# Kernel tuning notes

Hardware: AMD Instinct MI355X
Metric: run time of the kernel (lower is better)

The kernel has to match this reference:

```python
import jax, jax.numpy as jnp
import numpy as np

ANCHORS = np.array([[10.,13.],[16.,30.],[33.,23.],[30.,61.],[62.,45.],
                    [59.,119.],[116.,90.],[156.,198.],[373.,326.]], dtype=np.float32)
ANCHOR_MASK = [[6,7,8],[3,4,5],[0,1,2]]
INPUT_WH = np.array([320., 320.], dtype=np.float32)  # (W, H) == input_shape[::-1] (square)
IGNORE_THRESH = 0.5
NUM_CLASSES = 80
GRIDS = [10, 20, 40]
BATCH = 4


def _bce_logits(labels, logits):
    # tf.nn.sigmoid_cross_entropy_with_logits
    return jnp.maximum(logits, 0.0) - logits * labels + jnp.log1p(jnp.exp(-jnp.abs(logits)))


def _yolo_head(feats, anchors):
    gh, gw = feats.shape[1], feats.shape[2]
    gx = jnp.arange(gw, dtype=feats.dtype)
    gy = jnp.arange(gh, dtype=feats.dtype)
    # grid[..., 0] = x, grid[..., 1] = y ; shape [gh, gw, 1, 2]
    grid = jnp.stack(jnp.meshgrid(gx, gy), axis=-1)[:, :, None, :]
    box_xy = (jax.nn.sigmoid(feats[..., :2]) + grid) / jnp.array([gw, gh], feats.dtype)
    anc = jnp.asarray(anchors, feats.dtype).reshape(1, 1, 1, -1, 2)
    box_wh = jnp.exp(feats[..., 2:4]) * anc / jnp.asarray(INPUT_WH, feats.dtype)
    return grid, box_xy, box_wh


def _pairwise_iou(p, t):
    # p: [B,P,4] pred boxes (cx,cy,w,h); t: [B,N,4] true boxes -> iou [B,P,N]
    p_min = p[:, :, None, :2] - p[:, :, None, 2:4] * 0.5
    p_max = p[:, :, None, :2] + p[:, :, None, 2:4] * 0.5
    t_min = t[:, None, :, :2] - t[:, None, :, 2:4] * 0.5
    t_max = t[:, None, :, :2] + t[:, None, :, 2:4] * 0.5
    wh = jnp.maximum(jnp.minimum(p_max, t_max) - jnp.maximum(p_min, t_min), 0.0)
    inter = wh[..., 0] * wh[..., 1]
    p_area = p[:, :, None, 2] * p[:, :, None, 3]
    t_area = t[:, None, :, 2] * t[:, None, :, 3]
    return inter / (p_area + t_area - inter)


def _layer_loss(t, y, anchors, g):
    obj = t[..., 4:5]                      # [B,g,g,3,1]
    objb = obj != 0
    grid, pxy, pwh = _yolo_head(y, anchors)
    pred_box = jnp.concatenate([pxy, pwh], axis=-1)
    raw_true_xy = t[..., :2] * jnp.array([g, g], t.dtype) - grid
    anc = jnp.asarray(anchors, t.dtype).reshape(1, 1, 1, -1, 2)
    wh_scaled = t[..., 2:4] * jnp.asarray(INPUT_WH, t.dtype) / anc
    raw_true_wh = jnp.where(objb, jnp.log(jnp.where(objb, wh_scaled, 1.0)), 0.0)
    box_scale = 2.0 - t[..., 2:3] * t[..., 3:4]

    # ignore mask: masked pairwise IoU (all-slots, statically shaped; mask = objectness)
    B = t.shape[0]
    P = g * g * 3
    pb = pred_box.reshape(B, P, 4)
    tb = t[..., :4].reshape(B, P, 4)
    tmask = (t[..., 4] != 0).reshape(B, P)
    iou = _pairwise_iou(pb, tb)                         # [B,P,P]
    iou = jnp.where(tmask[:, None, :], iou, -jnp.inf)
    best_iou = jnp.max(iou, axis=-1)                    # -inf when no true boxes (matches empty reduce_max)
    ignore = (best_iou < IGNORE_THRESH).astype(t.dtype).reshape(obj.shape)

    xy_loss = obj * box_scale * _bce_logits(raw_true_xy, y[..., 0:2])
    wh_loss = obj * box_scale * 0.5 * jnp.square(raw_true_wh - y[..., 2:4])
    conf_loss = (obj + (1.0 - obj) * ignore) * _bce_logits(obj, y[..., 4:5])
    cls_loss = obj * _bce_logits(t[..., 5:], y[..., 5:])

    per_img = (xy_loss.sum((1, 2, 3, 4)) + wh_loss.sum((1, 2, 3, 4))
               + conf_loss.sum((1, 2, 3, 4)) + cls_loss.sum((1, 2, 3, 4)))
    return jnp.mean(per_img)


def setup_inputs() -> dict:
    key = jax.random.key(0)
    inp = {}
    for l, g in enumerate(GRIDS):
        k = jax.random.fold_in(key, l)
        k1, k2, k3, k4, k5 = jax.random.split(k, 5)
        xy = jax.random.uniform(k1, (BATCH, g, g, 3, 2), jnp.float32)
        wh = jax.random.uniform(k2, (BATCH, g, g, 3, 2), jnp.float32, 0.05, 0.9)
        obj = jax.random.bernoulli(k3, 0.02, (BATCH, g, g, 3, 1)).astype(jnp.float32)
        cls = jax.random.uniform(k4, (BATCH, g, g, 3, NUM_CLASSES), jnp.float32)
        inp[f"t{l}"] = jnp.concatenate([xy, wh, obj, cls], axis=-1)
        inp[f"y{l}"] = jax.random.normal(k5, (BATCH, g, g, 3, 5 + NUM_CLASSES), jnp.float32)
    return inp


def reference(t0, t1, t2, y0, y1, y2):
    targets = [t0, t1, t2]
    outputs = [y0, y1, y2]
    loss = jnp.float32(0.0)
    for l in range(3):
        loss = loss + _layer_loss(targets[l], outputs[l], ANCHORS[ANCHOR_MASK[l]], GRIDS[l])
    return loss
```

## Files before the change

kernel.cpp:

```cpp
#include <hip/hip_runtime.h>
#include <math.h>


#define NBLK 104
#define SCAP 512
#define NT4 535500

__device__ __constant__ float c_anc[3][3][2] = {
  {{116.f, 90.f}, {156.f, 198.f}, {373.f, 326.f}},
  {{ 30.f, 61.f}, { 62.f,  45.f}, { 59.f, 119.f}},
  {{ 10.f, 13.f}, { 16.f,  30.f}, { 33.f,  23.f}}};

__device__ __forceinline__ float bce_f(float label, float logit) {
    return fmaxf(logit, 0.0f) - logit * label + log1pf(expf(-fabsf(logit)));
}

__global__ __launch_bounds__(256) void k_scan(
    const float* __restrict__ t0, const float* __restrict__ y0,
    const float* __restrict__ t1, const float* __restrict__ y1,
    const float* __restrict__ t2, const float* __restrict__ y2,
    float* __restrict__ flag, float4* __restrict__ boxes,
    float* __restrict__ qbuf, int* __restrict__ done)
{
    int gid = blockIdx.x * 256 + threadIdx.x;
    if (gid == 0) *done = 0;
    int stride = gridDim.x * 256;
    for (int i = gid; i < 2 * NT4; i += stride) {
        bool isY = i >= NT4;
        int f4 = isY ? i - NT4 : i;
        const float* src; int rowBase, fi;
        if (f4 < 25500)       { src = isY ? y0 : t0; fi = f4 * 4;              rowBase = 0;    }
        else if (f4 < 127500) { src = isY ? y1 : t1; fi = (f4 - 25500) * 4;    rowBase = 1200; }
        else                  { src = isY ? y2 : t2; fi = (f4 - 127500) * 4;   rowBase = 6000; }
        float4 v = *(const float4*)(src + fi);
        float xs[4] = {v.x, v.y, v.z, v.w};
        #pragma unroll
        for (int c = 0; c < 4; ++c) {
            int f = fi + c;
            int row = f / 85;
            int ch  = f - row * 85;
            float x = xs[c];
            int grow = rowBase + row;
            if (!isY) {
                if (ch == 4) {
                    flag[grow] = x;
                    if (x != 0.0f) {
                        const float* tp = src + (size_t)row * 85;
                        boxes[grow] = make_float4(tp[0], tp[1], tp[2], tp[3]);
                    }
                }
            } else {
                if (ch < 5) qbuf[grow * 5 + ch] = x;
            }
        }
    }
}

template<int P, int G>
__device__ __forceinline__ float layer_block(
    const float* __restrict__ t, const float* __restrict__ y,
    int img, int chunk, int rowBase, const float (*anc)[2],
    const float* __restrict__ flag, const float4* __restrict__ boxes,
    const float* __restrict__ qbuf,
    float4* sbox, int* scount)
{
    const int gbase = rowBase + img * P;
    const float* fimg = flag + gbase;

    if (threadIdx.x == 0) *scount = 0;
    __syncthreads();
    const float4* fimg4 = (const float4*)fimg;
    for (int k4 = threadIdx.x; k4 < P / 4; k4 += 256) {
        float4 fv = fimg4[k4];
        float fs[4] = {fv.x, fv.y, fv.z, fv.w};
        #pragma unroll
        for (int c = 0; c < 4; ++c) {
            if (fs[c] != 0.0f) {
                int off = atomicAdd(scount, 1);
                if (off < SCAP) sbox[off] = boxes[gbase + k4 * 4 + c];
            }
        }
    }
    __syncthreads();
    int cnt = *scount; if (cnt > SCAP) cnt = SCAP;
    int cntPad = (cnt + 7) & ~7;
    for (int k = cnt + threadIdx.x; k < cntPad; k += 256)
        sbox[k] = make_float4(0.f, 0.f, 0.f, 0.f);
    __syncthreads();

    int pos = chunk * 256 + threadIdx.x;
    bool valid = pos < P;
    float acc = 0.0f, obj = 0.0f;
    if (valid) {
        const float* qp = qbuf + (size_t)(gbase + pos) * 5;
        float q0 = qp[0], q1 = qp[1], q2 = qp[2], q3 = qp[3], q4 = qp[4];
        obj = fimg[pos];
        int a = pos % 3, cell = pos / 3;
        int j = cell % G, i = cell / G;
        float aw = anc[a][0], ah = anc[a][1];
        float gi = (float)G;

        float px = (1.0f / (1.0f + expf(-q0)) + (float)j) / gi;
        float py = (1.0f / (1.0f + expf(-q1)) + (float)i) / gi;
        float pw = expf(q2) * aw * (1.0f / 320.0f);
        float ph = expf(q3) * ah * (1.0f / 320.0f);
        float phx = pw * 0.5f, phy = ph * 0.5f;
        float pminx = px - phx, pmaxx = px + phx;
        float pminy = py - phy, pmaxy = py + phy;
        float parea = pw * ph;

        float best = -INFINITY;
        for (int k0 = 0; k0 < cntPad; k0 += 8) {
            #pragma unroll
            for (int u = 0; u < 8; ++u) {
                float4 tb = sbox[k0 + u];
                float thx = tb.z * 0.5f, thy = tb.w * 0.5f;
                float wx = fminf(pmaxx, tb.x + thx) - fmaxf(pminx, tb.x - thx);
                float wy = fminf(pmaxy, tb.y + thy) - fmaxf(pminy, tb.y - thy);
                wx = fmaxf(wx, 0.0f);
                wy = fmaxf(wy, 0.0f);
                float inter = wx * wy;
                float iou = inter / (parea + tb.z * tb.w - inter);
                best = fmaxf(best, iou);
            }
        }
        float ignore = (best < 0.5f) ? 1.0f : 0.0f;
        float bce_c = fmaxf(q4, 0.0f) - q4 * obj + log1pf(expf(-fabsf(q4)));
        acc = (obj + (1.0f - obj) * ignore) * bce_c;
    }

    const float* tslab = t + (size_t)img * P * 85;
    const float* yslab = y + (size_t)img * P * 85;
    unsigned long long m = __ballot(valid && obj != 0.0f);
    int lane = threadIdx.x & 63;
    int waveBase = chunk * 256 + (threadIdx.x & ~63);
    while (m) {
        int b = __ffsll(m) - 1; m &= m - 1;
        int ppos = waveBase + b;
        const float* tp = tslab + (size_t)ppos * 85;
        const float* yp = yslab + (size_t)ppos * 85;
        float tv1 = tp[lane], yv1 = yp[lane];
        bool has2 = lane < 21;
        float tv2 = 0.f, yv2 = 0.f;
        if (has2) { tv2 = tp[lane + 64]; yv2 = yp[lane + 64]; }

        float tw = __shfl(tv1, 2, 64);
        float th = __shfl(tv1, 3, 64);
        float bs = 2.0f - tw * th;
        int a = ppos % 3, cell = ppos / 3;
        int jj = cell % G, ii = cell / G;
        float aw = anc[a][0], ah = anc[a][1];

        float term;
        if (lane == 0)      term = bs * bce_f(tv1 * (float)G - (float)jj, yv1);
        else if (lane == 1) term = bs * bce_f(tv1 * (float)G - (float)ii, yv1);
        else if (lane == 2) { float d = logf(tv1 * 320.0f / aw) - yv1; term = bs * 0.5f * d * d; }
        else if (lane == 3) { float d = logf(tv1 * 320.0f / ah) - yv1; term = bs * 0.5f * d * d; }
        else if (lane == 4) term = 0.0f;
        else                term = bce_f(tv1, yv1);
        if (has2) term += bce_f(tv2, yv2);
        acc += term;
    }
    return acc;
}

__global__ __launch_bounds__(256) void k_main(
    const float* __restrict__ t0, const float* __restrict__ y0,
    const float* __restrict__ t1, const float* __restrict__ y1,
    const float* __restrict__ t2, const float* __restrict__ y2,
    const float* __restrict__ flag, const float4* __restrict__ boxes,
    const float* __restrict__ qbuf,
    float* __restrict__ partials, int* __restrict__ done,
    float* __restrict__ out)
{
    __shared__ float4 sbox[SCAP];
    __shared__ int scount;
    int blk = blockIdx.x;

    float acc;
    if (blk < 8)       acc = layer_block< 300, 10>(t0, y0, blk >> 1, blk & 1, 0, c_anc[0], flag, boxes, qbuf, sbox, &scount);
    else if (blk < 28) { int r = blk - 8;  acc = layer_block<1200, 20>(t1, y1, r / 5,  r % 5,  1200, c_anc[1], flag, boxes, qbuf, sbox, &scount); }
    else               { int r = blk - 28; acc = layer_block<4800, 40>(t2, y2, r / 19, r % 19, 6000, c_anc[2], flag, boxes, qbuf, sbox, &scount); }

    float v = acc;
    #pragma unroll
    for (int o = 32; o > 0; o >>= 1) v += __shfl_down(v, o, 64);
    __shared__ float red[4];
    int lane = threadIdx.x & 63, w = threadIdx.x >> 6;
    if (lane == 0) red[w] = v;
    __syncthreads();

    if (threadIdx.x < 64) {
        int old = 0;
        if (threadIdx.x == 0) {
            float p = ((red[0] + red[1]) + (red[2] + red[3])) * 0.25f;
            __hip_atomic_store(&partials[blk], p, __ATOMIC_RELAXED, __HIP_MEMORY_SCOPE_AGENT);
            old = __hip_atomic_fetch_add(done, 1, __ATOMIC_ACQ_REL, __HIP_MEMORY_SCOPE_AGENT);
        }
        old = __shfl(old, 0, 64);
        if (old == NBLK - 1) {
            float s = 0.0f;
            if (lane < NBLK - 64)
                s = __hip_atomic_load(&partials[lane + 64], __ATOMIC_RELAXED, __HIP_MEMORY_SCOPE_AGENT);
            s += __hip_atomic_load(&partials[lane], __ATOMIC_RELAXED, __HIP_MEMORY_SCOPE_AGENT);
            #pragma unroll
            for (int o = 32; o > 0; o >>= 1) s += __shfl_down(s, o, 64);
            if (lane == 0) out[0] = s;
        }
    }
}

extern "C" void kernel_launch(void* const* d_in, const int* in_sizes, int n_in,
                              void* d_out, int out_size, void* d_ws, size_t ws_size,
                              hipStream_t stream) {
    const float* t0 = (const float*)d_in[0];
    const float* y0 = (const float*)d_in[1];
    const float* t1 = (const float*)d_in[2];
    const float* y1 = (const float*)d_in[3];
    const float* t2 = (const float*)d_in[4];
    const float* y2 = (const float*)d_in[5];

    float*  flag     = (float*)d_ws;
    float4* boxes    = (float4*)((char*)d_ws + 102400);
    float*  qbuf     = (float*)((char*)d_ws + 512000);
    float*  partials = (float*)((char*)d_ws + 1016064);
    int*    done     = (int*)((char*)d_ws + 1020160);
    float*  out      = (float*)d_out;

    k_scan<<<2048, 256, 0, stream>>>(t0, y0, t1, y1, t2, y2, flag, boxes, qbuf, done);
    k_main<<<NBLK, 256, 0, stream>>>(t0, y0, t1, y1, t2, y2, flag, boxes, qbuf, partials, done, out);
}
```

Baseline: 34.57 us.

## Fuse scan and main kernels into one cooperative launch with grid sync

Merges the scan pass and the loss pass into a single cooperative kernel of 512 blocks, separated by a grid-wide barrier, with only the first 104 blocks continuing into the loss phase. This removes one kernel launch and the inter-kernel gap. In exchange it adds cooperative-launch overhead and a grid barrier, and the scan now runs on 512 blocks instead of 2048.

```diff
diff --git a/kernel.cpp b/kernel.cpp
--- a/kernel.cpp
+++ b/kernel.cpp
@@ -1,10 +1,14 @@
 #include <hip/hip_runtime.h>
+#include <hip/hip_cooperative_groups.h>
 #include <math.h>
+
+namespace cg = cooperative_groups;
 
 
 #define NBLK 104
 #define SCAP 512
 #define NT4 535500
+#define GRID_BLOCKS 512
 
 __device__ __constant__ float c_anc[3][3][2] = {
   {{116.f, 90.f}, {156.f, 198.f}, {373.f, 326.f}},
@@ -15,16 +19,126 @@
     return fmaxf(logit, 0.0f) - logit * label + log1pf(expf(-fabsf(logit)));
 }
 
-__global__ __launch_bounds__(256) void k_scan(
+template<int P, int G>
+__device__ __forceinline__ float layer_block(
+    const float* __restrict__ t, const float* __restrict__ y,
+    int img, int chunk, int rowBase, const float (*anc)[2],
+    const float* __restrict__ flag, const float4* __restrict__ boxes,
+    const float* __restrict__ qbuf,
+    float4* sbox, int* scount)
+{
+    const int gbase = rowBase + img * P;
+    const float* fimg = flag + gbase;
+
+    if (threadIdx.x == 0) *scount = 0;
+    __syncthreads();
+    const float4* fimg4 = (const float4*)fimg;
+    for (int k4 = threadIdx.x; k4 < P / 4; k4 += 256) {
+        float4 fv = fimg4[k4];
+        float fs[4] = {fv.x, fv.y, fv.z, fv.w};
+        #pragma unroll
+        for (int c = 0; c < 4; ++c) {
+            if (fs[c] != 0.0f) {
+                int off = atomicAdd(scount, 1);
+                if (off < SCAP) sbox[off] = boxes[gbase + k4 * 4 + c];
+            }
+        }
+    }
+    __syncthreads();
+    int cnt = *scount; if (cnt > SCAP) cnt = SCAP;
+    int cntPad = (cnt + 7) & ~7;
+    for (int k = cnt + threadIdx.x; k < cntPad; k += 256)
+        sbox[k] = make_float4(0.f, 0.f, 0.f, 0.f);
+    __syncthreads();
+
+    int pos = chunk * 256 + threadIdx.x;
+    bool valid = pos < P;
+    float acc = 0.0f, obj = 0.0f;
+    if (valid) {
+        const float* qp = qbuf + (size_t)(gbase + pos) * 5;
+        float q0 = qp[0], q1 = qp[1], q2 = qp[2], q3 = qp[3], q4 = qp[4];
+        obj = fimg[pos];
+        int a = pos % 3, cell = pos / 3;
+        int j = cell % G, i = cell / G;
+        float aw = anc[a][0], ah = anc[a][1];
+        float gi = (float)G;
+
+        float px = (1.0f / (1.0f + expf(-q0)) + (float)j) / gi;
+        float py = (1.0f / (1.0f + expf(-q1)) + (float)i) / gi;
+        float pw = expf(q2) * aw * (1.0f / 320.0f);
+        float ph = expf(q3) * ah * (1.0f / 320.0f);
+        float phx = pw * 0.5f, phy = ph * 0.5f;
+        float pminx = px - phx, pmaxx = px + phx;
+        float pminy = py - phy, pmaxy = py + phy;
+        float parea = pw * ph;
+
+        float best = -INFINITY;
+        for (int k0 = 0; k0 < cntPad; k0 += 8) {
+            #pragma unroll
+            for (int u = 0; u < 8; ++u) {
+                float4 tb = sbox[k0 + u];
+                float thx = tb.z * 0.5f, thy = tb.w * 0.5f;
+                float wx = fminf(pmaxx, tb.x + thx) - fmaxf(pminx, tb.x - thx);
+                float wy = fminf(pmaxy, tb.y + thy) - fmaxf(pminy, tb.y - thy);
+                wx = fmaxf(wx, 0.0f);
+                wy = fmaxf(wy, 0.0f);
+                float inter = wx * wy;
+                float iou = inter / (parea + tb.z * tb.w - inter);
+                best = fmaxf(best, iou);
+            }
+        }
+        float ignore = (best < 0.5f) ? 1.0f : 0.0f;
+        float bce_c = fmaxf(q4, 0.0f) - q4 * obj + log1pf(expf(-fabsf(q4)));
+        acc = (obj + (1.0f - obj) * ignore) * bce_c;
+    }
+
+    const float* tslab = t + (size_t)img * P * 85;
+    const float* yslab = y + (size_t)img * P * 85;
+    unsigned long long m = __ballot(valid && obj != 0.0f);
+    int lane = threadIdx.x & 63;
+    int waveBase = chunk * 256 + (threadIdx.x & ~63);
+    while (m) {
+        int b = __ffsll(m) - 1; m &= m - 1;
+        int ppos = waveBase + b;
+        const float* tp = tslab + (size_t)ppos * 85;
+        const float* yp = yslab + (size_t)ppos * 85;
+        float tv1 = tp[lane], yv1 = yp[lane];
+        bool has2 = lane < 21;
+        float tv2 = 0.f, yv2 = 0.f;
+        if (has2) { tv2 = tp[lane + 64]; yv2 = yp[lane + 64]; }
+
+        float tw = __shfl(tv1, 2, 64);
+        float th = __shfl(tv1, 3, 64);
+        float bs = 2.0f - tw * th;
+        int a = ppos % 3, cell = ppos / 3;
+        int jj = cell % G, ii = cell / G;
+        float aw = anc[a][0], ah = anc[a][1];
+
+        float term;
+        if (lane == 0)      term = bs * bce_f(tv1 * (float)G - (float)jj, yv1);
+        else if (lane == 1) term = bs * bce_f(tv1 * (float)G - (float)ii, yv1);
+        else if (lane == 2) { float d = logf(tv1 * 320.0f / aw) - yv1; term = bs * 0.5f * d * d; }
+        else if (lane == 3) { float d = logf(tv1 * 320.0f / ah) - yv1; term = bs * 0.5f * d * d; }
+        else if (lane == 4) term = 0.0f;
+        else                term = bce_f(tv1, yv1);
+        if (has2) term += bce_f(tv2, yv2);
+        acc += term;
+    }
+    return acc;
+}
+
+__global__ __launch_bounds__(256) void k_fused(
     const float* __restrict__ t0, const float* __restrict__ y0,
     const float* __restrict__ t1, const float* __restrict__ y1,
     const float* __restrict__ t2, const float* __restrict__ y2,
     float* __restrict__ flag, float4* __restrict__ boxes,
-    float* __restrict__ qbuf, int* __restrict__ done)
+    float* __restrict__ qbuf, float* __restrict__ partials,
+    int* __restrict__ done, float* __restrict__ out)
 {
     int gid = blockIdx.x * 256 + threadIdx.x;
-    if (gid == 0) *done = 0;
-    int stride = gridDim.x * 256;
+    if (gid == 0)
+        __hip_atomic_store(done, 0, __ATOMIC_RELAXED, __HIP_MEMORY_SCOPE_AGENT);
+    const int stride = GRID_BLOCKS * 256;
     for (int i = gid; i < 2 * NT4; i += stride) {
         bool isY = i >= NT4;
         int f4 = isY ? i - NT4 : i;
@@ -54,125 +168,11 @@
             }
         }
     }
-}
-
-template<int P, int G>
-__device__ __forceinline__ float layer_block(
-    const float* __restrict__ t, const float* __restrict__ y,
-    int img, int chunk, int rowBase, const float (*anc)[2],
-    const float* __restrict__ flag, const float4* __restrict__ boxes,
-    const float* __restrict__ qbuf,
-    float4* sbox, int* scount)
-{
-    const int gbase = rowBase + img * P;
-    const float* fimg = flag + gbase;
-
-    if (threadIdx.x == 0) *scount = 0;
-    __syncthreads();
-    const float4* fimg4 = (const float4*)fimg;
-    for (int k4 = threadIdx.x; k4 < P / 4; k4 += 256) {
-        float4 fv = fimg4[k4];
-        float fs[4] = {fv.x, fv.y, fv.z, fv.w};
-        #pragma unroll
-        for (int c = 0; c < 4; ++c) {
-            if (fs[c] != 0.0f) {
-                int off = atomicAdd(scount, 1);
-                if (off < SCAP) sbox[off] = boxes[gbase + k4 * 4 + c];
-            }
-        }
-    }
-    __syncthreads();
-    int cnt = *scount; if (cnt > SCAP) cnt = SCAP;
-    int cntPad = (cnt + 7) & ~7;
-    for (int k = cnt + threadIdx.x; k < cntPad; k += 256)
-        sbox[k] = make_float4(0.f, 0.f, 0.f, 0.f);
-    __syncthreads();
-
-    int pos = chunk * 256 + threadIdx.x;
-    bool valid = pos < P;
-    float acc = 0.0f, obj = 0.0f;
-    if (valid) {
-        const float* qp = qbuf + (size_t)(gbase + pos) * 5;
-        float q0 = qp[0], q1 = qp[1], q2 = qp[2], q3 = qp[3], q4 = qp[4];
-        obj = fimg[pos];
-        int a = pos % 3, cell = pos / 3;
-        int j = cell % G, i = cell / G;
-        float aw = anc[a][0], ah = anc[a][1];
-        float gi = (float)G;
-
-        float px = (1.0f / (1.0f + expf(-q0)) + (float)j) / gi;
-        float py = (1.0f / (1.0f + expf(-q1)) + (float)i) / gi;
-        float pw = expf(q2) * aw * (1.0f / 320.0f);
-        float ph = expf(q3) * ah * (1.0f / 320.0f);
-        float phx = pw * 0.5f, phy = ph * 0.5f;
-        float pminx = px - phx, pmaxx = px + phx;
-        float pminy = py - phy, pmaxy = py + phy;
-        float parea = pw * ph;
-
-        float best = -INFINITY;
-        for (int k0 = 0; k0 < cntPad; k0 += 8) {
-            #pragma unroll
-            for (int u = 0; u < 8; ++u) {
-                float4 tb = sbox[k0 + u];
-                float thx = tb.z * 0.5f, thy = tb.w * 0.5f;
-                float wx = fminf(pmaxx, tb.x + thx) - fmaxf(pminx, tb.x - thx);
-                float wy = fminf(pmaxy, tb.y + thy) - fmaxf(pminy, tb.y - thy);
-                wx = fmaxf(wx, 0.0f);
-                wy = fmaxf(wy, 0.0f);
-                float inter = wx * wy;
-                float iou = inter / (parea + tb.z * tb.w - inter);
-                best = fmaxf(best, iou);
-            }
-        }
-        float ignore = (best < 0.5f) ? 1.0f : 0.0f;
-        float bce_c = fmaxf(q4, 0.0f) - q4 * obj + log1pf(expf(-fabsf(q4)));
-        acc = (obj + (1.0f - obj) * ignore) * bce_c;
-    }
-
-    const float* tslab = t + (size_t)img * P * 85;
-    const float* yslab = y + (size_t)img * P * 85;
-    unsigned long long m = __ballot(valid && obj != 0.0f);
-    int lane = threadIdx.x & 63;
-    int waveBase = chunk * 256 + (threadIdx.x & ~63);
-    while (m) {
-        int b = __ffsll(m) - 1; m &= m - 1;
-        int ppos = waveBase + b;
-        const float* tp = tslab + (size_t)ppos * 85;
-        const float* yp = yslab + (size_t)ppos * 85;
-        float tv1 = tp[lane], yv1 = yp[lane];
-        bool has2 = lane < 21;
-        float tv2 = 0.f, yv2 = 0.f;
-        if (has2) { tv2 = tp[lane + 64]; yv2 = yp[lane + 64]; }
-
-        float tw = __shfl(tv1, 2, 64);
-        float th = __shfl(tv1, 3, 64);
-        float bs = 2.0f - tw * th;
-        int a = ppos % 3, cell = ppos / 3;
-        int jj = cell % G, ii = cell / G;
-        float aw = anc[a][0], ah = anc[a][1];
-
-        float term;
-        if (lane == 0)      term = bs * bce_f(tv1 * (float)G - (float)jj, yv1);
-        else if (lane == 1) term = bs * bce_f(tv1 * (float)G - (float)ii, yv1);
-        else if (lane == 2) { float d = logf(tv1 * 320.0f / aw) - yv1; term = bs * 0.5f * d * d; }
-        else if (lane == 3) { float d = logf(tv1 * 320.0f / ah) - yv1; term = bs * 0.5f * d * d; }
-        else if (lane == 4) term = 0.0f;
-        else                term = bce_f(tv1, yv1);
-        if (has2) term += bce_f(tv2, yv2);
-        acc += term;
-    }
-    return acc;
-}
-
-__global__ __launch_bounds__(256) void k_main(
-    const float* __restrict__ t0, const float* __restrict__ y0,
-    const float* __restrict__ t1, const float* __restrict__ y1,
-    const float* __restrict__ t2, const float* __restrict__ y2,
-    const float* __restrict__ flag, const float4* __restrict__ boxes,
-    const float* __restrict__ qbuf,
-    float* __restrict__ partials, int* __restrict__ done,
-    float* __restrict__ out)
-{
+
+    cg::this_grid().sync();
+
+    if (blockIdx.x >= NBLK) return;
+
     __shared__ float4 sbox[SCAP];
     __shared__ int scount;
     int blk = blockIdx.x;
@@ -227,6 +227,9 @@
     int*    done     = (int*)((char*)d_ws + 1020160);
     float*  out      = (float*)d_out;
 
-    k_scan<<<2048, 256, 0, stream>>>(t0, y0, t1, y1, t2, y2, flag, boxes, qbuf, done);
-    k_main<<<NBLK, 256, 0, stream>>>(t0, y0, t1, y1, t2, y2, flag, boxes, qbuf, partials, done, out);
-}
+    void* args[] = { (void*)&t0, (void*)&y0, (void*)&t1, (void*)&y1,
+                     (void*)&t2, (void*)&y2, (void*)&flag, (void*)&boxes,
+                     (void*)&qbuf, (void*)&partials, (void*)&done, (void*)&out };
+    hipLaunchCooperativeKernel((const void*)k_fused, dim3(GRID_BLOCKS), dim3(256),
+                               args, 0, stream);
+}
```

Measured after the change: 104.8 us. 203% more time.
